# Performance work log

Measured on AMD Instinct MI355X. Metric: run time of the kernel, lower is better.

The kernel has to match this reference:

```python
import jax, jax.numpy as jnp
import numpy as np
import math

D = 256; H = 8; DH = 32; FF = 2048; L = 6; B = 4; S = 1022


def _pe(n, d):
    pos = np.arange(n)[:, None]
    div = np.exp(np.arange(0, d, 2) * (-math.log(10000.0) / d))
    pe = np.zeros((n, d), np.float32)
    pe[:, 0::2] = np.sin(pos * div)
    pe[:, 1::2] = np.cos(pos * div)
    return jnp.asarray(pe)


def _ln(x, g, b):
    mu = x.mean(-1, keepdims=True)
    v = ((x - mu) ** 2).mean(-1, keepdims=True)
    return (x - mu) / jnp.sqrt(v + 1e-5) * g + b


def _forward(x, cls1, cls2, Wqkv, bqkv, Wo, bo, ln1_g, ln1_b, W1, b1, W2, b2, ln2_g, ln2_b, idx, pad):
    n = x.shape[1] + 2  # insert cls1 and cls2 tokens
    h = jnp.stack([jnp.concatenate([cls1, x[i, :idx[i]], cls2, x[i, idx[i]:]], axis=0) for i in range(B)])
    h = h + _pe(n, D)[None]  # [B,N,D]
    # block-diagonal two-segment mask per sample (additive bias form)
    pos = np.arange(n)
    bias = []
    for i in range(B):
        v1 = pos <= idx[i]
        v2 = (pos > idx[i]) & (pos < n - pad[i])
        allowed = np.outer(v1, v1) | np.outer(v2, v2)
        bias.append(np.where(allowed, 0.0, -1e9).astype(np.float32))
    bias = jnp.asarray(np.stack(bias))[:, None]  # [B,1,N,N]
    scale = 1.0 / math.sqrt(DH)
    for l in range(L):
        qkv = h @ Wqkv[l].T + bqkv[l]  # [B,N,3D]
        q, k, v = jnp.split(qkv, 3, axis=-1)
        q = q.reshape(B, n, H, DH).transpose(0, 2, 1, 3)
        k = k.reshape(B, n, H, DH).transpose(0, 2, 1, 3)
        v = v.reshape(B, n, H, DH).transpose(0, 2, 1, 3)
        scores = jnp.einsum('bhqd,bhkd->bhqk', q, k) * scale + bias
        p = jax.nn.softmax(scores, axis=-1)
        a = jnp.einsum('bhqk,bhkd->bhqd', p, v).transpose(0, 2, 1, 3).reshape(B, n, D)
        h = _ln(h + a @ Wo[l].T + bo[l], ln1_g[l], ln1_b[l])
        ff = jax.nn.relu(h @ W1[l].T + b1[l]) @ W2[l].T + b2[l]
        h = _ln(h + ff, ln2_g[l], ln2_b[l])
    # cls token outputs: position 0 (cls1) and position idx+1 (cls2)
    return jnp.stack([jnp.stack([h[i, 0], h[i, idx[i] + 1]]) for i in range(B)])  # [4,2,256]


def setup_inputs():
    key = jax.random.key(0)
    ks = jax.random.split(key, 8)
    s = 0.02
    return {
        'x': jax.random.normal(ks[0], (B, S, D), jnp.float32),
        'mask': jnp.zeros((1,), jnp.bool_),  # unused by the original forward
        'indices': jnp.array([[500, 600, 400, 300], [0, 0, 0, 0]], jnp.int32),
        'cls1': jax.random.uniform(ks[1], (1, D), jnp.float32),
        'cls2': jax.random.uniform(ks[2], (1, D), jnp.float32),
        'Wqkv': jax.random.normal(ks[3], (L, 3 * D, D), jnp.float32) * s,
        'bqkv': jnp.zeros((L, 3 * D), jnp.float32),
        'Wo': jax.random.normal(ks[4], (L, D, D), jnp.float32) * s,
        'bo': jnp.zeros((L, D), jnp.float32),
        'ln1_g': jnp.ones((L, D), jnp.float32),
        'ln1_b': jnp.zeros((L, D), jnp.float32),
        'W1': jax.random.normal(ks[5], (L, FF, D), jnp.float32) * s,
        'b1': jnp.zeros((L, FF), jnp.float32),
        'W2': jax.random.normal(ks[6], (L, D, FF), jnp.float32) * s,
        'b2': jnp.zeros((L, D), jnp.float32),
        'ln2_g': jnp.ones((L, D), jnp.float32),
        'ln2_b': jnp.zeros((L, D), jnp.float32),
    }


def reference(x, mask, indices, cls1, cls2, Wqkv, bqkv, Wo, bo, ln1_g, ln1_b, W1, b1, W2, b2, ln2_g, ln2_b):
    ind = np.asarray(indices)
    idx = [int(t) for t in ind[0]]
    pad = [int(t) for t in ind[1]]
    return _forward(x, cls1, cls2, Wqkv, bqkv, Wo, bo, ln1_g, ln1_b, W1, b1, W2, b2, ln2_g, ln2_b, idx, pad)
```

## Files before the change

### kernel.cpp

```cpp
#include <hip/hip_runtime.h>
#include <hip/hip_bf16.h>
#include <math.h>

typedef __hip_bfloat16 bf16;
typedef short bf16x8 __attribute__((ext_vector_type(8)));
typedef float f32x4 __attribute__((ext_vector_type(4)));

#define D_MODEL 256
#define NTOK 1024
#define SEQ 1022
#define BATCH 4
#define NLAYER 6

__device__ inline void gload_lds16(const void* g, void* l) {
    __builtin_amdgcn_global_load_lds(
        (const __attribute__((address_space(1))) void*)g,
        (__attribute__((address_space(3))) void*)l, 16, 0, 0);
}

__global__ __launch_bounds__(256) void cast_kernel(
    const float* __restrict__ in, bf16* __restrict__ out, int n)
{
    int i = (blockIdx.x * 256 + threadIdx.x) * 4;
    if (i >= n) return;
    f32x4 v = *(const f32x4*)(in + i);
    out[i + 0] = __float2bfloat16(v[0]);
    out[i + 1] = __float2bfloat16(v[1]);
    out[i + 2] = __float2bfloat16(v[2]);
    out[i + 3] = __float2bfloat16(v[3]);
}

__global__ __launch_bounds__(256) void embed_kernel(
    const float* __restrict__ x, const float* __restrict__ cls1,
    const float* __restrict__ cls2, const int* __restrict__ ind,
    float* __restrict__ h, bf16* __restrict__ hb)
{
    int i = blockIdx.x * 256 + threadIdx.x;
    int d = i & 255;
    int pos = (i >> 8) & 1023;
    int b = i >> 18;
    int idx = ind[b];
    float v;
    if (pos == 0) v = cls1[d];
    else if (pos == idx + 1) v = cls2[d];
    else if (pos <= idx) v = x[(b * SEQ + pos - 1) * D_MODEL + d];
    else v = x[(b * SEQ + pos - 2) * D_MODEL + d];
    int p = d >> 1;
    float freq = expf(-(float)p * (logf(10000.0f) / 128.0f));
    float ang = (float)pos * freq;
    v += (d & 1) ? cosf(ang) : sinf(ang);
    h[i] = v;
    hb[i] = __float2bfloat16(v);
}

template<int MR, int NR, int RELU, int HAS_RES, int WF32, int WBF16, int WVT>
__global__ __launch_bounds__(256) void mfma_gemm(
    const bf16* __restrict__ A, const bf16* __restrict__ W,
    const float* __restrict__ bias, const float* __restrict__ R,
    float* __restrict__ Cf, bf16* __restrict__ Cb, bf16* __restrict__ vTb,
    int M, int N, int K)
{
    constexpr int BM = MR * 32, BN = NR * 32;
    constexpr int ACH = BM * 4;
    constexpr int BCH = BN * 4;
    __shared__ bf16 As[2][BM * 32];
    __shared__ bf16 Bs[2][BN * 32];
    const int ntile = N / BN;
    const int bx = blockIdx.x % ntile, by = blockIdx.x / ntile;
    const int row0 = by * BM, col0 = bx * BN;
    const int tid = threadIdx.x, lane = tid & 63, wave = tid >> 6;
    const int wr = wave >> 1, wc = wave & 1;
    const int l15 = lane & 15, l4 = lane >> 4;

    f32x4 acc[MR][NR];
    #pragma unroll
    for (int m = 0; m < MR; ++m)
        #pragma unroll
        for (int n = 0; n < NR; ++n) acc[m][n] = (f32x4)0.0f;

    const int nk = K / 32;

    auto stage = [&](int buf, int t) {
        const int k0 = t * 32;
        #pragma unroll
        for (int p = 0; p < ACH / 256; ++p) {
            const int cbase = p * 256 + wave * 64;
            const int chunk = cbase + lane;
            const int r = chunk >> 2, c = chunk & 3;
            gload_lds16(A + (size_t)(row0 + r) * K + k0 + c * 8, &As[buf][cbase * 8]);
        }
        #pragma unroll
        for (int p = 0; p < BCH / 256; ++p) {
            const int cbase = p * 256 + wave * 64;
            const int chunk = cbase + lane;
            const int r = chunk >> 2, c = chunk & 3;
            gload_lds16(W + (size_t)(col0 + r) * K + k0 + c * 8, &Bs[buf][cbase * 8]);
        }
    };

    stage(0, 0);
    __syncthreads();
    int cur = 0;
    for (int t = 0; t < nk; ++t) {
        if (t + 1 < nk) stage(cur ^ 1, t + 1);
        bf16x8 af[MR], bfr[NR];
        #pragma unroll
        for (int m = 0; m < MR; ++m)
            af[m] = *(const bf16x8*)&As[cur][(wr * MR * 16 + m * 16 + l15) * 32 + l4 * 8];
        #pragma unroll
        for (int n = 0; n < NR; ++n)
            bfr[n] = *(const bf16x8*)&Bs[cur][(wc * NR * 16 + n * 16 + l15) * 32 + l4 * 8];
        #pragma unroll
        for (int m = 0; m < MR; ++m)
            #pragma unroll
            for (int n = 0; n < NR; ++n)
                acc[m][n] = __builtin_amdgcn_mfma_f32_16x16x32_bf16(af[m], bfr[n], acc[m][n], 0, 0, 0);
        __syncthreads();
        cur ^= 1;
    }

    #pragma unroll
    for (int m = 0; m < MR; ++m) {
        #pragma unroll
        for (int n = 0; n < NR; ++n) {
            const int col = col0 + wc * NR * 16 + n * 16 + l15;
            const float bv = bias[col];
            #pragma unroll
            for (int r = 0; r < 4; ++r) {
                const int row = row0 + wr * MR * 16 + m * 16 + l4 * 4 + r;
                float v = acc[m][n][r] + bv;
                if (HAS_RES) v += R[(size_t)row * N + col];
                if (RELU) v = fmaxf(v, 0.0f);
                if (WF32) Cf[(size_t)row * N + col] = v;
                if (WBF16) {
                    if (WVT && col >= 512) {
                        const int hh = (col >> 5) - 16, d = col & 31;
                        const int bb = row >> 10, tt = row & 1023;
                        vTb[(((size_t)bb * 8 + hh) * 32 + d) * 1024 + tt] = __float2bfloat16(v);
                    } else {
                        Cb[(size_t)row * N + col] = __float2bfloat16(v);
                    }
                }
            }
        }
    }
}

__global__ __launch_bounds__(256) void attn_mfma_kernel(
    const bf16* __restrict__ qkvb, const bf16* __restrict__ vT,
    bf16* __restrict__ att, const int* __restrict__ ind)
{
    __shared__ bf16 Ps[4][16][72];
    const int qt = blockIdx.x & 15;
    const int hh = (blockIdx.x >> 4) & 7;
    const int b  = blockIdx.x >> 7;
    const int idx = ind[b];
    const int segEnd = NTOK - ind[4 + b];
    const int tid = threadIdx.x, lane = tid & 63, wave = tid >> 6;
    const int l15 = lane & 15, l4 = lane >> 4;
    const int q0 = qt * 64 + wave * 16;
    const size_t tokbase = (size_t)b * NTOK;
    const bf16* vTh = vT + (((size_t)b * 8 + hh) * 32) * 1024;
    const float scale = 0.17677669529663687f;

    const bf16x8 qfrag = *(const bf16x8*)(qkvb + (tokbase + q0 + l15) * 768 + hh * 32 + l4 * 8);

    f32x4 acc_o[2];
    acc_o[0] = (f32x4)0.0f; acc_o[1] = (f32x4)0.0f;
    float mrun[4], lrun[4];
    bool v1q[4], v2q[4];
    #pragma unroll
    for (int r = 0; r < 4; ++r) {
        mrun[r] = -1e30f; lrun[r] = 0.0f;
        const int qg = q0 + l4 * 4 + r;
        v1q[r] = (qg <= idx);
        v2q[r] = (qg > idx) && (qg < segEnd);
    }

    const int kbeg = (q0 <= idx) ? 0 : (idx + 1);
    const int kend = (q0 + 15 > idx) ? segEnd : (idx + 1);

    for (int k0 = (kbeg & ~63); k0 < kend; k0 += 64) {
        f32x4 sc[4];
        #pragma unroll
        for (int kt = 0; kt < 4; ++kt) {
            const bf16x8 kf = *(const bf16x8*)
                (qkvb + (tokbase + k0 + kt * 16 + l15) * 768 + 256 + hh * 32 + l4 * 8);
            sc[kt] = __builtin_amdgcn_mfma_f32_16x16x32_bf16(qfrag, kf, (f32x4)0.0f, 0, 0, 0);
        }
        float mloc[4] = {-1e30f, -1e30f, -1e30f, -1e30f};
        #pragma unroll
        for (int kt = 0; kt < 4; ++kt) {
            const int k = k0 + kt * 16 + l15;
            const bool v1k = (k <= idx);
            const bool v2k = (k > idx) && (k < segEnd);
            #pragma unroll
            for (int r = 0; r < 4; ++r) {
                const bool ok = (v1q[r] && v1k) || (v2q[r] && v2k);
                const float s = ok ? sc[kt][r] * scale : -1e30f;
                sc[kt][r] = s;
                mloc[r] = fmaxf(mloc[r], s);
            }
        }
        #pragma unroll
        for (int r = 0; r < 4; ++r) {
            mloc[r] = fmaxf(mloc[r], __shfl_xor(mloc[r], 1));
            mloc[r] = fmaxf(mloc[r], __shfl_xor(mloc[r], 2));
            mloc[r] = fmaxf(mloc[r], __shfl_xor(mloc[r], 4));
            mloc[r] = fmaxf(mloc[r], __shfl_xor(mloc[r], 8));
            const float mnew = fmaxf(mrun[r], mloc[r]);
            const float c = __expf(mrun[r] - mnew);
            mrun[r] = mnew;
            mloc[r] = c;
        }
        float psum[4] = {0.0f, 0.0f, 0.0f, 0.0f};
        #pragma unroll
        for (int kt = 0; kt < 4; ++kt) {
            #pragma unroll
            for (int r = 0; r < 4; ++r) {
                const float s = sc[kt][r];
                const float p = (s > -5e29f) ? __expf(s - mrun[r]) : 0.0f;
                psum[r] += p;
                Ps[wave][l4 * 4 + r][kt * 16 + l15] = __float2bfloat16(p);
            }
        }
        #pragma unroll
        for (int r = 0; r < 4; ++r) {
            float ps = psum[r];
            ps += __shfl_xor(ps, 1); ps += __shfl_xor(ps, 2);
            ps += __shfl_xor(ps, 4); ps += __shfl_xor(ps, 8);
            lrun[r] = lrun[r] * mloc[r] + ps;
            acc_o[0][r] *= mloc[r];
            acc_o[1][r] *= mloc[r];
        }
        #pragma unroll
        for (int ks = 0; ks < 2; ++ks) {
            const bf16x8 pa = *(const bf16x8*)&Ps[wave][l15][ks * 32 + l4 * 8];
            #pragma unroll
            for (int dt = 0; dt < 2; ++dt) {
                const bf16x8 vb = *(const bf16x8*)
                    (vTh + (size_t)(dt * 16 + l15) * 1024 + k0 + ks * 32 + l4 * 8);
                acc_o[dt] = __builtin_amdgcn_mfma_f32_16x16x32_bf16(pa, vb, acc_o[dt], 0, 0, 0);
            }
        }
    }

    #pragma unroll
    for (int r = 0; r < 4; ++r) {
        const float invl = (lrun[r] > 0.0f) ? (1.0f / lrun[r]) : 0.0f;
        const int qg = q0 + l4 * 4 + r;
        bf16* op = att + (tokbase + qg) * 256 + hh * 32 + l15;
        op[0]  = __float2bfloat16(acc_o[0][r] * invl);
        op[16] = __float2bfloat16(acc_o[1][r] * invl);
    }
}

__global__ __launch_bounds__(256) void ln_kernel(
    const float* __restrict__ X, const float* __restrict__ g,
    const float* __restrict__ bb, float* __restrict__ Y, bf16* __restrict__ Yb)
{
    const int row = blockIdx.x * 4 + (threadIdx.x >> 6);
    const int lane = threadIdx.x & 63;
    const f32x4 xv = *(const f32x4*)(X + (size_t)row * 256 + lane * 4);
    float s = (xv[0] + xv[1]) + (xv[2] + xv[3]);
    #pragma unroll
    for (int off = 32; off >= 1; off >>= 1) s += __shfl_xor(s, off);
    const float mu = s * (1.0f / 256.0f);
    f32x4 dv;
    float s2 = 0.0f;
    #pragma unroll
    for (int e = 0; e < 4; ++e) { dv[e] = xv[e] - mu; s2 += dv[e] * dv[e]; }
    #pragma unroll
    for (int off = 32; off >= 1; off >>= 1) s2 += __shfl_xor(s2, off);
    const float inv = 1.0f / sqrtf(s2 * (1.0f / 256.0f) + 1e-5f);
    const f32x4 gv = *(const f32x4*)(g + lane * 4);
    const f32x4 bv = *(const f32x4*)(bb + lane * 4);
    f32x4 y;
    bf16x8 yb2;
    short sh[4];
    #pragma unroll
    for (int e = 0; e < 4; ++e) {
        y[e] = dv[e] * inv * gv[e] + bv[e];
        sh[e] = __builtin_bit_cast(short, __float2bfloat16(y[e]));
    }
    *(f32x4*)(Y + (size_t)row * 256 + lane * 4) = y;
    typedef short short4v __attribute__((ext_vector_type(4)));
    short4v pack; pack[0] = sh[0]; pack[1] = sh[1]; pack[2] = sh[2]; pack[3] = sh[3];
    *(short4v*)((short*)Yb + (size_t)row * 256 + lane * 4) = pack;
    (void)yb2;
}

__global__ __launch_bounds__(256) void gather_kernel(
    const float* __restrict__ h, const int* __restrict__ ind, float* __restrict__ out)
{
    int b = blockIdx.x;
    int tid = threadIdx.x;
    out[(b * 2 + 0) * 256 + tid] = h[(b * NTOK + 0) * 256 + tid];
    out[(b * 2 + 1) * 256 + tid] = h[(b * NTOK + ind[b] + 1) * 256 + tid];
}

extern "C" void kernel_launch(void* const* d_in, const int* in_sizes, int n_in,
                              void* d_out, int out_size, void* d_ws, size_t ws_size,
                              hipStream_t stream)
{
    const float* x    = (const float*)d_in[0];
    const int*   ind  = (const int*)d_in[2];
    const float* cls1 = (const float*)d_in[3];
    const float* cls2 = (const float*)d_in[4];
    const float* Wqkv = (const float*)d_in[5];
    const float* bqkv = (const float*)d_in[6];
    const float* Wo   = (const float*)d_in[7];
    const float* bo   = (const float*)d_in[8];
    const float* g1   = (const float*)d_in[9];
    const float* be1  = (const float*)d_in[10];
    const float* W1   = (const float*)d_in[11];
    const float* bf1  = (const float*)d_in[12];
    const float* W2   = (const float*)d_in[13];
    const float* bf2  = (const float*)d_in[14];
    const float* g2   = (const float*)d_in[15];
    const float* be2  = (const float*)d_in[16];
    float* out = (float*)d_out;

    float* ws   = (float*)d_ws;
    float* h    = ws;
    float* tmp  = h + 1048576;
    bf16* hb    = (bf16*)(tmp + 1048576);
    bf16* qkvb  = hb + 1048576;
    bf16* vTb   = qkvb + 3145728;
    bf16* attb  = vTb + 1048576;
    bf16* ffb   = attb + 1048576;
    bf16* wqkvb = ffb + 8388608;
    bf16* wob   = wqkvb + 1179648;
    bf16* w1b   = wob + 393216;
    bf16* w2b   = w1b + 3145728;

    const int M = BATCH * NTOK;

    cast_kernel<<<1152, 256, 0, stream>>>(Wqkv, wqkvb, 1179648);
    cast_kernel<<<384,  256, 0, stream>>>(Wo,   wob,   393216);
    cast_kernel<<<3072, 256, 0, stream>>>(W1,   w1b,   3145728);
    cast_kernel<<<3072, 256, 0, stream>>>(W2,   w2b,   3145728);

    embed_kernel<<<M, 256, 0, stream>>>(x, cls1, cls2, ind, h, hb);

    for (int l = 0; l < NLAYER; ++l) {
        const bf16*  Wqkv_l = wqkvb + (size_t)l * 768 * 256;
        const float* bqkv_l = bqkv + (size_t)l * 768;
        const bf16*  Wo_l   = wob + (size_t)l * 256 * 256;
        const float* bo_l   = bo + (size_t)l * 256;
        const float* g1_l   = g1 + (size_t)l * 256;
        const float* be1_l  = be1 + (size_t)l * 256;
        const bf16*  W1_l   = w1b + (size_t)l * 2048 * 256;
        const float* bf1_l  = bf1 + (size_t)l * 2048;
        const bf16*  W2_l   = w2b + (size_t)l * 256 * 2048;
        const float* bf2_l  = bf2 + (size_t)l * 256;
        const float* g2_l   = g2 + (size_t)l * 256;
        const float* be2_l  = be2 + (size_t)l * 256;

        mfma_gemm<4, 4, 0, 0, 0, 1, 1><<<(M / 128) * (768 / 128), 256, 0, stream>>>(
            hb, Wqkv_l, bqkv_l, nullptr, nullptr, qkvb, vTb, M, 768, 256);
        attn_mfma_kernel<<<BATCH * 8 * 16, 256, 0, stream>>>(qkvb, vTb, attb, ind);
        mfma_gemm<2, 2, 0, 1, 1, 0, 0><<<(M / 64) * (256 / 64), 256, 0, stream>>>(
            attb, Wo_l, bo_l, h, tmp, nullptr, nullptr, M, 256, 256);
        ln_kernel<<<M / 4, 256, 0, stream>>>(tmp, g1_l, be1_l, h, hb);
        mfma_gemm<4, 4, 1, 0, 0, 1, 0><<<(M / 128) * (2048 / 128), 256, 0, stream>>>(
            hb, W1_l, bf1_l, nullptr, nullptr, ffb, nullptr, M, 2048, 256);
        mfma_gemm<2, 2, 0, 1, 1, 0, 0><<<(M / 64) * (256 / 64), 256, 0, stream>>>(
            ffb, W2_l, bf2_l, h, tmp, nullptr, nullptr, M, 256, 2048);
        ln_kernel<<<M / 4, 256, 0, stream>>>(tmp, g2_l, be2_l, h, hb);
    }

    gather_kernel<<<BATCH, 256, 0, stream>>>(h, ind, out);
}
```

Measured before the change: 591.6 us.

## Fuse output-projection and FFN2 GEMMs with residual add and LayerNorm

Adds a GEMM kernel that computes full 16-row by 256-column output tiles, with K split across four waves and reduced through shared memory. It then applies bias, the residual add and LayerNorm in the same kernel, writing fp32 and bf16 hidden states directly. This removes the separate LN launches and the fp32 tmp round trip. The QKV and FFN1 GEMM tiles also shrink from 128 to 64 rows to launch more blocks. In exchange, the fused kernel reads A and W straight from global memory without LDS staging, so each block rereads the whole weight matrix, and each block uses about 66KB of LDS, which may limit occupancy.

Result: no change. 594.1 us (+0.4%).

```diff
diff --git a/kernel.cpp b/kernel.cpp
--- a/kernel.cpp
+++ b/kernel.cpp
@@ -4,6 +4,7 @@
 
 typedef __hip_bfloat16 bf16;
 typedef short bf16x8 __attribute__((ext_vector_type(8)));
+typedef short short4v __attribute__((ext_vector_type(4)));
 typedef float f32x4 __attribute__((ext_vector_type(4)));
 
 #define D_MODEL 256
@@ -146,6 +147,89 @@
     }
 }
 
+template<int K>
+__global__ __launch_bounds__(256) void gemm256_ln_kernel(
+    const bf16* __restrict__ A, const bf16* __restrict__ W,
+    const float* __restrict__ bias, const float* __restrict__ g,
+    const float* __restrict__ be, float* __restrict__ h, bf16* __restrict__ hb)
+{
+    constexpr int KW = K / 4;
+    constexpr int NSTEP = KW / 32;
+    __shared__ float part[4][16][260];
+    const int tid = threadIdx.x, lane = tid & 63, wave = tid >> 6;
+    const int l15 = lane & 15, l4 = lane >> 4;
+    const int row0 = blockIdx.x * 16;
+    const int kbase = wave * KW;
+
+    f32x4 acc[16];
+    #pragma unroll
+    for (int n = 0; n < 16; ++n) acc[n] = (f32x4)0.0f;
+
+    #pragma unroll
+    for (int s = 0; s < NSTEP; ++s) {
+        const int kk = kbase + s * 32;
+        const bf16x8 af = *(const bf16x8*)(A + (size_t)(row0 + l15) * K + kk + l4 * 8);
+        #pragma unroll
+        for (int n = 0; n < 16; ++n) {
+            const bf16x8 bf_ = *(const bf16x8*)(W + (size_t)(n * 16 + l15) * K + kk + l4 * 8);
+            acc[n] = __builtin_amdgcn_mfma_f32_16x16x32_bf16(af, bf_, acc[n], 0, 0, 0);
+        }
+    }
+    #pragma unroll
+    for (int n = 0; n < 16; ++n)
+        #pragma unroll
+        for (int r = 0; r < 4; ++r)
+            part[wave][l4 * 4 + r][n * 16 + l15] = acc[n][r];
+    __syncthreads();
+
+    const int row = tid >> 4, colg = tid & 15;
+    f32x4 v[4];
+    #pragma unroll
+    for (int e = 0; e < 4; ++e) {
+        v[e] = *(const f32x4*)&part[0][row][colg * 16 + e * 4];
+        #pragma unroll
+        for (int w = 1; w < 4; ++w)
+            v[e] += *(const f32x4*)&part[w][row][colg * 16 + e * 4];
+    }
+    float* hrow = h + (size_t)(row0 + row) * 256 + colg * 16;
+    float s1 = 0.0f;
+    #pragma unroll
+    for (int e = 0; e < 4; ++e) {
+        const f32x4 bv = *(const f32x4*)(bias + colg * 16 + e * 4);
+        const f32x4 rv = *(const f32x4*)(hrow + e * 4);
+        v[e] += bv + rv;
+        s1 += (v[e][0] + v[e][1]) + (v[e][2] + v[e][3]);
+    }
+    #pragma unroll
+    for (int off = 8; off >= 1; off >>= 1) s1 += __shfl_xor(s1, off);
+    const float mu = s1 * (1.0f / 256.0f);
+    float s2 = 0.0f;
+    #pragma unroll
+    for (int e = 0; e < 4; ++e) {
+        #pragma unroll
+        for (int q = 0; q < 4; ++q) { const float d = v[e][q] - mu; s2 += d * d; }
+    }
+    #pragma unroll
+    for (int off = 8; off >= 1; off >>= 1) s2 += __shfl_xor(s2, off);
+    const float inv = 1.0f / sqrtf(s2 * (1.0f / 256.0f) + 1e-5f);
+
+    short* hbrow = (short*)hb + (size_t)(row0 + row) * 256 + colg * 16;
+    #pragma unroll
+    for (int e = 0; e < 4; ++e) {
+        const f32x4 gv = *(const f32x4*)(g + colg * 16 + e * 4);
+        const f32x4 bv2 = *(const f32x4*)(be + colg * 16 + e * 4);
+        f32x4 y;
+        short4v pk;
+        #pragma unroll
+        for (int q = 0; q < 4; ++q) {
+            y[q] = (v[e][q] - mu) * inv * gv[q] + bv2[q];
+            pk[q] = __builtin_bit_cast(short, __float2bfloat16(y[q]));
+        }
+        *(f32x4*)(hrow + e * 4) = y;
+        *(short4v*)(hbrow + e * 4) = pk;
+    }
+}
+
 __global__ __launch_bounds__(256) void attn_mfma_kernel(
     const bf16* __restrict__ qkvb, const bf16* __restrict__ vT,
     bf16* __restrict__ att, const int* __restrict__ ind)
@@ -253,41 +337,6 @@
         op[0]  = __float2bfloat16(acc_o[0][r] * invl);
         op[16] = __float2bfloat16(acc_o[1][r] * invl);
     }
-}
-
-__global__ __launch_bounds__(256) void ln_kernel(
-    const float* __restrict__ X, const float* __restrict__ g,
-    const float* __restrict__ bb, float* __restrict__ Y, bf16* __restrict__ Yb)
-{
-    const int row = blockIdx.x * 4 + (threadIdx.x >> 6);
-    const int lane = threadIdx.x & 63;
-    const f32x4 xv = *(const f32x4*)(X + (size_t)row * 256 + lane * 4);
-    float s = (xv[0] + xv[1]) + (xv[2] + xv[3]);
-    #pragma unroll
-    for (int off = 32; off >= 1; off >>= 1) s += __shfl_xor(s, off);
-    const float mu = s * (1.0f / 256.0f);
-    f32x4 dv;
-    float s2 = 0.0f;
-    #pragma unroll
-    for (int e = 0; e < 4; ++e) { dv[e] = xv[e] - mu; s2 += dv[e] * dv[e]; }
-    #pragma unroll
-    for (int off = 32; off >= 1; off >>= 1) s2 += __shfl_xor(s2, off);
-    const float inv = 1.0f / sqrtf(s2 * (1.0f / 256.0f) + 1e-5f);
-    const f32x4 gv = *(const f32x4*)(g + lane * 4);
-    const f32x4 bv = *(const f32x4*)(bb + lane * 4);
-    f32x4 y;
-    bf16x8 yb2;
-    short sh[4];
-    #pragma unroll
-    for (int e = 0; e < 4; ++e) {
-        y[e] = dv[e] * inv * gv[e] + bv[e];
-        sh[e] = __builtin_bit_cast(short, __float2bfloat16(y[e]));
-    }
-    *(f32x4*)(Y + (size_t)row * 256 + lane * 4) = y;
-    typedef short short4v __attribute__((ext_vector_type(4)));
-    short4v pack; pack[0] = sh[0]; pack[1] = sh[1]; pack[2] = sh[2]; pack[3] = sh[3];
-    *(short4v*)((short*)Yb + (size_t)row * 256 + lane * 4) = pack;
-    (void)yb2;
 }
 
 __global__ __launch_bounds__(256) void gather_kernel(
@@ -323,8 +372,7 @@
 
     float* ws   = (float*)d_ws;
     float* h    = ws;
-    float* tmp  = h + 1048576;
-    bf16* hb    = (bf16*)(tmp + 1048576);
+    bf16* hb    = (bf16*)(h + 1048576);
     bf16* qkvb  = hb + 1048576;
     bf16* vTb   = qkvb + 3145728;
     bf16* attb  = vTb + 1048576;
@@ -357,17 +405,15 @@
         const float* g2_l   = g2 + (size_t)l * 256;
         const float* be2_l  = be2 + (size_t)l * 256;
 
-        mfma_gemm<4, 4, 0, 0, 0, 1, 1><<<(M / 128) * (768 / 128), 256, 0, stream>>>(
+        mfma_gemm<2, 4, 0, 0, 0, 1, 1><<<(M / 64) * (768 / 128), 256, 0, stream>>>(
             hb, Wqkv_l, bqkv_l, nullptr, nullptr, qkvb, vTb, M, 768, 256);
         attn_mfma_kernel<<<BATCH * 8 * 16, 256, 0, stream>>>(qkvb, vTb, attb, ind);
-        mfma_gemm<2, 2, 0, 1, 1, 0, 0><<<(M / 64) * (256 / 64), 256, 0, stream>>>(
-            attb, Wo_l, bo_l, h, tmp, nullptr, nullptr, M, 256, 256);
-        ln_kernel<<<M / 4, 256, 0, stream>>>(tmp, g1_l, be1_l, h, hb);
-        mfma_gemm<4, 4, 1, 0, 0, 1, 0><<<(M / 128) * (2048 / 128), 256, 0, stream>>>(
+        gemm256_ln_kernel<256><<<M / 16, 256, 0, stream>>>(
+            attb, Wo_l, bo_l, g1_l, be1_l, h, hb);
+        mfma_gemm<2, 4, 1, 0, 0, 1, 0><<<(M / 64) * (2048 / 128), 256, 0, stream>>>(
             hb, W1_l, bf1_l, nullptr, nullptr, ffb, nullptr, M, 2048, 256);
-        mfma_gemm<2, 2, 0, 1, 1, 0, 0><<<(M / 64) * (256 / 64), 256, 0, stream>>>(
-            ffb, W2_l, bf2_l, h, tmp, nullptr, nullptr, M, 256, 2048);
-        ln_kernel<<<M / 4, 256, 0, stream>>>(tmp, g2_l, be2_l, h, hb);
+        gemm256_ln_kernel<2048><<<M / 16, 256, 0, stream>>>(
+            ffb, W2_l, bf2_l, g2_l, be2_l, h, hb);
     }
 
     gather_kernel<<<BATCH, 256, 0, stream>>>(h, ind, out);
```
